# Performance work log

Measured on AMD Instinct MI355X. Metric: run time of the kernel, lower is better.

Reference implementation:

```python
import jax, jax.numpy as jnp
import numpy as np

C = 256          # in_channels == inter_channels (structurally required)
B, H, W = 16, 64, 64


def setup_inputs() -> dict:
    key = jax.random.key(0)
    ks = jax.random.split(key, 10)
    s = 1.0 / np.sqrt(C)
    x = jax.random.normal(ks[0], (B, C, H, W), dtype=jnp.float32)
    # theta / phi: 1x1 convs, stored as [out, in]
    theta_w = jax.random.normal(ks[1], (C, C), dtype=jnp.float32) * s
    theta_b = jax.random.normal(ks[2], (C,), dtype=jnp.float32) * s
    phi_w = jax.random.normal(ks[3], (C, C), dtype=jnp.float32) * s
    phi_b = jax.random.normal(ks[4], (C,), dtype=jnp.float32) * s
    # grouped conv: Conv2d(C, 2C, kernel=(C,1), groups=C).
    # torch weight [2C, 1, C, 1] with group-major out-channel order -> [C groups, 2 per group, C taps]
    gw = jax.random.normal(ks[5], (C, 2, C), dtype=jnp.float32) * s
    gb = jax.random.normal(ks[6], (C, 2), dtype=jnp.float32) * s
    # dim_adjust: 1x1 conv 2C -> C, stored as [C, 2C]
    dw = jax.random.normal(ks[7], (C, 2 * C), dtype=jnp.float32) * (1.0 / np.sqrt(2 * C))
    db = jax.random.normal(ks[8], (C,), dtype=jnp.float32) * (1.0 / np.sqrt(2 * C))
    return {"x": x, "theta_w": theta_w, "theta_b": theta_b,
            "phi_w": phi_w, "phi_b": phi_b,
            "gw": gw, "gb": gb, "dw": dw, "db": db}


def reference(x, theta_w, theta_b, phi_w, phi_b, gw, gb, dw, db):
    b, c, h, w = x.shape
    xf = x.reshape(b, c, h * w)                                   # [B,C,HW]
    theta = jnp.einsum('oc,bcn->bon', theta_w, xf) + theta_b[:, None]  # [B,Ci,HW]
    phi = jnp.einsum('oc,bcn->bon', phi_w, xf) + phi_b[:, None]        # [B,Ci,HW]
    f = jnp.einsum('bon,bpn->bop', theta, phi)                    # [B,Ci,Ci] channel similarity
    # grouped conv: group g sees channel g of f over its 'spatial' axis (length Ci),
    # producing 2 outputs per group via a full-height dot product.
    g = jnp.einsum('bgk,gjk->bgj', f, gw) + gb                    # [B,C,2]
    g = jax.nn.relu(g).reshape(b, 2 * c)                          # [B,2C]
    out = jnp.einsum('bo,co->bc', g, dw) + db                     # [B,C] 1x1 conv
    return out[:, :, None, None]                                  # [B,C,1,1]
```

## Files before the change

### kernel.cpp

```cpp
#include <hip/hip_runtime.h>


#define CC  256
#define NB  16
#define HWN 4096

typedef __attribute__((ext_vector_type(4))) float f32x4;
typedef __attribute__((ext_vector_type(8))) short bf16x8;

__device__ inline unsigned short f2bf(float f) {
  unsigned u = __float_as_uint(f);
  u += 0x7fff + ((u >> 16) & 1);
  return (unsigned short)(u >> 16);
}
__device__ inline float bf2f(unsigned u) { return __uint_as_float(u << 16); }

__global__ __launch_bounds__(1024, 4) void k_gram(const float* __restrict__ x,
                                                  unsigned short* __restrict__ slab,
                                                  float* __restrict__ S) {
  const int ks = blockIdx.x, b = blockIdx.y;
  const float* xb = x + (size_t)b * CC * HWN;
  __shared__ unsigned short As[2][256 * 64];

  const int tid = threadIdx.x, w = tid >> 6, lane = tid & 63;
  const int quad = lane >> 4, m15 = lane & 15;
  const int srow = tid >> 4;
  const int scol = (tid & 15) << 2;
  const int sg = scol >> 3, so = scol & 7;

  f32x4 acc[16];
  #pragma unroll
  for (int i = 0; i < 16; ++i) acc[i] = (f32x4){0.f, 0.f, 0.f, 0.f};
  float rs[4] = {0.f, 0.f, 0.f, 0.f};

  const int k0 = ks * 256;
  float4 ld[4];
  #pragma unroll
  for (int p = 0; p < 4; ++p)
    ld[p] = *(const float4*)(xb + (size_t)(p * 64 + srow) * HWN + k0 + scol);
  #pragma unroll
  for (int p = 0; p < 4; ++p) {
    const int row = p * 64 + srow;
    rs[p] += ld[p].x + ld[p].y + ld[p].z + ld[p].w;
    *(ushort4*)&As[0][row * 64 + ((sg ^ (row & 7)) << 3) + so] =
        make_ushort4(f2bf(ld[p].x), f2bf(ld[p].y), f2bf(ld[p].z), f2bf(ld[p].w));
  }
  __syncthreads();

  #pragma unroll
  for (int i = 0; i < 4; ++i) {
    const int cur = i & 1;
    if (i < 3) {
      const int kc = k0 + (i + 1) * 64;
      #pragma unroll
      for (int p = 0; p < 4; ++p)
        ld[p] = *(const float4*)(xb + (size_t)(p * 64 + srow) * HWN + kc + scol);
    }
    const int rowa = 16 * w + m15;
    #pragma unroll
    for (int kkg = 0; kkg < 8; kkg += 4) {
      const int ga = (kkg + quad) ^ (m15 & 7);
      bf16x8 af = *(const bf16x8*)&As[cur][rowa * 64 + ga * 8];
      #pragma unroll
      for (int ct = 0; ct < 16; ++ct) {
        bf16x8 bfr = *(const bf16x8*)&As[cur][(16 * ct + m15) * 64 + ga * 8];
        acc[ct] = __builtin_amdgcn_mfma_f32_16x16x32_bf16(af, bfr, acc[ct], 0, 0, 0);
      }
    }
    if (i < 3) {
      #pragma unroll
      for (int p = 0; p < 4; ++p) {
        const int row = p * 64 + srow;
        rs[p] += ld[p].x + ld[p].y + ld[p].z + ld[p].w;
        *(ushort4*)&As[1 - cur][row * 64 + ((sg ^ (row & 7)) << 3) + so] =
            make_ushort4(f2bf(ld[p].x), f2bf(ld[p].y), f2bf(ld[p].z), f2bf(ld[p].w));
      }
    }
    __syncthreads();
  }

  unsigned short* sb = slab + ((size_t)(ks * 16 + b) << 16) + w * 4096 + lane;
  #pragma unroll
  for (int ct = 0; ct < 16; ++ct)
    #pragma unroll
    for (int reg = 0; reg < 4; ++reg)
      sb[(ct * 4 + reg) * 64] = f2bf(acc[ct][reg]);

  #pragma unroll
  for (int p = 0; p < 4; ++p) {
    float v = rs[p];
    v += __shfl_xor(v, 1);
    v += __shfl_xor(v, 2);
    v += __shfl_xor(v, 4);
    v += __shfl_xor(v, 8);
    if ((tid & 15) == 0) atomicAdd(&S[b * 256 + p * 64 + srow], v);
  }
}

__global__ __launch_bounds__(256) void k_reduce(const unsigned short* __restrict__ slab,
                                                unsigned short* __restrict__ Gh) {
  const int t = blockIdx.x * 256 + threadIdx.x;
  const int b = t >> 13;
  const int o = (t & 8191) << 3;
  float s[8];
  #pragma unroll
  for (int i = 0; i < 8; ++i) s[i] = 0.f;
  #pragma unroll
  for (int ks = 0; ks < 16; ++ks) {
    const uint4 v = *(const uint4*)(slab + (((size_t)(ks * 16 + b)) << 16) + o);
    s[0] += bf2f(v.x & 0xffffu); s[1] += bf2f(v.x >> 16);
    s[2] += bf2f(v.y & 0xffffu); s[3] += bf2f(v.y >> 16);
    s[4] += bf2f(v.z & 0xffffu); s[5] += bf2f(v.z >> 16);
    s[6] += bf2f(v.w & 0xffffu); s[7] += bf2f(v.w >> 16);
  }
  const int wv = o >> 12, rem = o & 4095;
  const int ctreg = rem >> 6, lane6 = rem & 63;
  const int ct = ctreg >> 2, reg = ctreg & 3;
  const int quad = lane6 >> 4, m0 = lane6 & 15;
  const int row = 16 * wv + 4 * quad + reg;
  const int col = 16 * ct + m0;
  uint4 ov;
  ov.x = (unsigned)f2bf(s[0]) | ((unsigned)f2bf(s[1]) << 16);
  ov.y = (unsigned)f2bf(s[2]) | ((unsigned)f2bf(s[3]) << 16);
  ov.z = (unsigned)f2bf(s[4]) | ((unsigned)f2bf(s[5]) << 16);
  ov.w = (unsigned)f2bf(s[6]) | ((unsigned)f2bf(s[7]) << 16);
  *(uint4*)(Gh + (((size_t)b) << 16) + row * 256 + col) = ov;
}

__global__ __launch_bounds__(256) void k_mid(const float* __restrict__ gw,
                                             const float* __restrict__ pw,
                                             const float* __restrict__ pb,
                                             const float* __restrict__ tw,
                                             const float* __restrict__ S,
                                             unsigned short* __restrict__ Qh,
                                             float* __restrict__ E,
                                             float* __restrict__ U,
                                             float* __restrict__ V) {
  __shared__ float sm[512];
  const int tid = threadIdx.x, blk = blockIdx.x;
  if (blk < 512) {
    const int rj = blk;
    sm[tid] = gw[rj * 256 + tid];
    __syncthreads();
    float q = 0.f;
    for (int p = 0; p < 256; ++p) q += sm[p] * pw[p * 256 + tid];
    Qh[rj * 256 + tid] = f2bf(q);
    sm[256 + tid] = sm[tid] * pb[tid];
    __syncthreads();
    for (int s = 128; s > 0; s >>= 1) {
      if (tid < s) sm[256 + tid] += sm[256 + tid + s];
      __syncthreads();
    }
    if (tid == 0) E[rj] = sm[256];
  } else {
    const int m = blk - 512;
    const int b = m & 15, mat = m >> 4;
    const float* Wm = mat ? pw : tw;
    float* outp = mat ? V : U;
    sm[tid] = S[b * 256 + tid];
    __syncthreads();
    const int l = tid & 15, oh = tid >> 4;
    #pragma unroll
    for (int oc = 0; oc < 16; ++oc) {
      const int o = oc * 16 + oh;
      float a = 0.f;
      #pragma unroll
      for (int j = 0; j < 16; ++j)
        a += Wm[o * 256 + l * 16 + j] * sm[l * 16 + j];
      a += __shfl_xor(a, 1);
      a += __shfl_xor(a, 2);
      a += __shfl_xor(a, 4);
      a += __shfl_xor(a, 8);
      if (l == 0) outp[b * 256 + o] = a;
    }
  }
}

__global__ __launch_bounds__(512) void k_p(const unsigned short* __restrict__ Gh,
                                           const unsigned short* __restrict__ Qh,
                                           const float* __restrict__ tw,
                                           const float* __restrict__ gw,
                                           const float* __restrict__ U,
                                           const float* __restrict__ V,
                                           const float* __restrict__ E,
                                           const float* __restrict__ tb,
                                           const float* __restrict__ gb,
                                           float* __restrict__ GR) {
  const int rjt = blockIdx.x, b = blockIdx.y;
  const int rj0 = rjt * 32;
  const int tid = threadIdx.x, w = tid >> 6, lane = tid & 63;
  const int quad = lane >> 4, m15 = lane & 15;
  const unsigned short* Gb = Gh + ((size_t)b << 16);

  f32x4 acc[2][2];
  #pragma unroll
  for (int mt = 0; mt < 2; ++mt) {
    acc[mt][0] = (f32x4){0.f, 0.f, 0.f, 0.f};
    acc[mt][1] = (f32x4){0.f, 0.f, 0.f, 0.f};
  }

  #pragma unroll
  for (int s = 0; s < 8; ++s) {
    const int kb = s * 32 + quad * 8;
    bf16x8 bq0 = *(const bf16x8*)(Qh + (rj0 + m15) * 256 + kb);
    bf16x8 bq1 = *(const bf16x8*)(Qh + (rj0 + 16 + m15) * 256 + kb);
    #pragma unroll
    for (int mt = 0; mt < 2; ++mt) {
      bf16x8 ag = *(const bf16x8*)(Gb + (32 * w + 16 * mt + m15) * 256 + kb);
      acc[mt][0] = __builtin_amdgcn_mfma_f32_16x16x32_bf16(ag, bq0, acc[mt][0], 0, 0, 0);
      acc[mt][1] = __builtin_amdgcn_mfma_f32_16x16x32_bf16(ag, bq1, acc[mt][1], 0, 0, 0);
    }
  }

  __shared__ float sred[32 * 8];
  __shared__ float sred2[32];
  #pragma unroll
  for (int nt = 0; nt < 2; ++nt) {
    const int rj = rj0 + 16 * nt + m15;
    const int r = rj >> 1;
    float p = 0.f;
    #pragma unroll
    for (int mt = 0; mt < 2; ++mt)
      #pragma unroll
      for (int reg = 0; reg < 4; ++reg)
        p += acc[mt][nt][reg] * tw[r * 256 + 32 * w + 16 * mt + quad * 4 + reg];
    p += __shfl_xor(p, 16);
    p += __shfl_xor(p, 32);
    if (quad == 0) sred[(16 * nt + m15) * 8 + w] = p;
  }
  {
    const int oi = tid >> 4, seg = tid & 15;
    const int rj = rj0 + oi;
    float p2 = 0.f;
    #pragma unroll
    for (int i = 0; i < 16; ++i) {
      const int cp = seg * 16 + i;
      p2 += gw[rj * 256 + cp] * V[b * 256 + cp];
    }
    p2 += __shfl_xor(p2, 1);
    p2 += __shfl_xor(p2, 2);
    p2 += __shfl_xor(p2, 4);
    p2 += __shfl_xor(p2, 8);
    if (seg == 0) sred2[oi] = p2;
  }
  __syncthreads();
  if (tid < 32) {
    const int rj = rj0 + tid, r = rj >> 1;
    float v = 0.f;
    #pragma unroll
    for (int k = 0; k < 8; ++k) v += sred[tid * 8 + k];
    const float tbr = tb[r];
    const float bias = tbr * sred2[tid] +
                       (U[b * 256 + r] + 4096.0f * tbr) * E[rj] + gb[rj];
    GR[b * 512 + rj] = fmaxf(v + bias, 0.f);
  }
}

__global__ __launch_bounds__(256) void k_out(const float* __restrict__ GR,
                                             const float* __restrict__ dw,
                                             const float* __restrict__ db,
                                             float* __restrict__ out) {
  const int cch = blockIdx.x, b = blockIdx.y, tid = threadIdx.x;
  __shared__ float gl[512];
  gl[tid] = GR[b * 512 + tid];
  gl[256 + tid] = GR[b * 512 + 256 + tid];
  __syncthreads();
  const int cl = tid >> 4, l = tid & 15;
  const int c = cch * 16 + cl;
  float a = 0.f;
  #pragma unroll 8
  for (int i = 0; i < 32; ++i) {
    const int o = i * 16 + l;
    a += gl[o] * dw[c * 512 + o];
  }
  a += __shfl_xor(a, 1);
  a += __shfl_xor(a, 2);
  a += __shfl_xor(a, 4);
  a += __shfl_xor(a, 8);
  if (l == 0) out[b * 256 + c] = a + db[c];
}

extern "C" void kernel_launch(void* const* d_in, const int* in_sizes, int n_in,
                              void* d_out, int out_size, void* d_ws, size_t ws_size,
                              hipStream_t stream) {
  const float* x  = (const float*)d_in[0];
  const float* tw = (const float*)d_in[1];
  const float* tb = (const float*)d_in[2];
  const float* pw = (const float*)d_in[3];
  const float* pb = (const float*)d_in[4];
  const float* gw = (const float*)d_in[5];
  const float* gb = (const float*)d_in[6];
  const float* dw = (const float*)d_in[7];
  const float* db = (const float*)d_in[8];
  float* out = (float*)d_out;

  unsigned short* slab = (unsigned short*)d_ws;
  unsigned short* Gh   = slab + ((size_t)256 << 16);
  unsigned short* Qh   = Gh + ((size_t)16 << 16);
  float* S  = (float*)(Qh + 512 * 256);
  float* E  = S + NB * 256;
  float* U  = E + 512;
  float* V  = U + NB * 256;
  float* GR = V + NB * 256;

  hipMemsetAsync(S, 0, NB * 256 * sizeof(float), stream);
  k_gram<<<dim3(16, 16), 1024, 0, stream>>>(x, slab, S);
  k_reduce<<<512, 256, 0, stream>>>(slab, Gh);
  k_mid<<<544, 256, 0, stream>>>(gw, pw, pb, tw, S, Qh, E, U, V);
  k_p<<<dim3(16, NB), 512, 0, stream>>>(Gh, Qh, tw, gw, U, V, E, tb, gb, GR);
  k_out<<<dim3(16, NB), 256, 0, stream>>>(GR, dw, db, out);
}
```

Before: 168.1 us.

## Exploit Gram symmetry, double K-split, and fuse reduce with mid kernel

The Gram kernel now computes only the upper-triangular 16x16 tiles of the symmetric channel matrix, doubles the K-split to 32 chunks so more blocks fill the GPU, and writes compact per-split partials and row sums instead of using atomics. The reduce and mid stages are merged into one launch that also mirrors tiles to rebuild the full matrix, and the memset is dropped. k_p is retiled to smaller blocks with more of them. The gain should come from fewer MFMAs, better occupancy and fewer launches, at the cost of twice as many partial slabs to reduce and wave-level load imbalance in the triangular loop.

```diff
diff --git a/kernel.cpp b/kernel.cpp
--- a/kernel.cpp
+++ b/kernel.cpp
@@ -4,6 +4,8 @@
 #define CC  256
 #define NB  16
 #define HWN 4096
+#define KSPLIT 32
+#define NPAIR 136
 
 typedef __attribute__((ext_vector_type(4))) float f32x4;
 typedef __attribute__((ext_vector_type(8))) short bf16x8;
@@ -17,7 +19,7 @@
 
 __global__ __launch_bounds__(1024, 4) void k_gram(const float* __restrict__ x,
                                                   unsigned short* __restrict__ slab,
-                                                  float* __restrict__ S) {
+                                                  float* __restrict__ Spart) {
   const int ks = blockIdx.x, b = blockIdx.y;
   const float* xb = x + (size_t)b * CC * HWN;
   __shared__ unsigned short As[2][256 * 64];
@@ -33,7 +35,7 @@
   for (int i = 0; i < 16; ++i) acc[i] = (f32x4){0.f, 0.f, 0.f, 0.f};
   float rs[4] = {0.f, 0.f, 0.f, 0.f};
 
-  const int k0 = ks * 256;
+  const int k0 = ks * 128;
   float4 ld[4];
   #pragma unroll
   for (int p = 0; p < 4; ++p)
@@ -48,43 +50,47 @@
   __syncthreads();
 
   #pragma unroll
-  for (int i = 0; i < 4; ++i) {
-    const int cur = i & 1;
-    if (i < 3) {
-      const int kc = k0 + (i + 1) * 64;
+  for (int i = 0; i < 2; ++i) {
+    if (i < 1) {
       #pragma unroll
       for (int p = 0; p < 4; ++p)
-        ld[p] = *(const float4*)(xb + (size_t)(p * 64 + srow) * HWN + kc + scol);
+        ld[p] = *(const float4*)(xb + (size_t)(p * 64 + srow) * HWN + k0 + 64 + scol);
     }
     const int rowa = 16 * w + m15;
     #pragma unroll
     for (int kkg = 0; kkg < 8; kkg += 4) {
       const int ga = (kkg + quad) ^ (m15 & 7);
-      bf16x8 af = *(const bf16x8*)&As[cur][rowa * 64 + ga * 8];
+      bf16x8 af = *(const bf16x8*)&As[i][rowa * 64 + ga * 8];
       #pragma unroll
       for (int ct = 0; ct < 16; ++ct) {
-        bf16x8 bfr = *(const bf16x8*)&As[cur][(16 * ct + m15) * 64 + ga * 8];
+        if (ct < w) continue;
+        bf16x8 bfr = *(const bf16x8*)&As[i][(16 * ct + m15) * 64 + ga * 8];
         acc[ct] = __builtin_amdgcn_mfma_f32_16x16x32_bf16(af, bfr, acc[ct], 0, 0, 0);
       }
     }
-    if (i < 3) {
+    if (i < 1) {
       #pragma unroll
       for (int p = 0; p < 4; ++p) {
         const int row = p * 64 + srow;
         rs[p] += ld[p].x + ld[p].y + ld[p].z + ld[p].w;
-        *(ushort4*)&As[1 - cur][row * 64 + ((sg ^ (row & 7)) << 3) + so] =
+        *(ushort4*)&As[1][row * 64 + ((sg ^ (row & 7)) << 3) + so] =
             make_ushort4(f2bf(ld[p].x), f2bf(ld[p].y), f2bf(ld[p].z), f2bf(ld[p].w));
       }
     }
     __syncthreads();
   }
 
-  unsigned short* sb = slab + ((size_t)(ks * 16 + b) << 16) + w * 4096 + lane;
-  #pragma unroll
-  for (int ct = 0; ct < 16; ++ct)
-    #pragma unroll
-    for (int reg = 0; reg < 4; ++reg)
-      sb[(ct * 4 + reg) * 64] = f2bf(acc[ct][reg]);
+  const int off_w = 16 * w - (w * (w - 1)) / 2;
+  unsigned short* sbase = slab + ((size_t)(ks * 16 + b) * NPAIR) * 256;
+  #pragma unroll
+  for (int ct = 0; ct < 16; ++ct) {
+    if (ct < w) continue;
+    const int pid = off_w + (ct - w);
+    uint2 ov;
+    ov.x = (unsigned)f2bf(acc[ct][0]) | ((unsigned)f2bf(acc[ct][1]) << 16);
+    ov.y = (unsigned)f2bf(acc[ct][2]) | ((unsigned)f2bf(acc[ct][3]) << 16);
+    *(uint2*)(sbase + pid * 256 + lane * 4) = ov;
+  }
 
   #pragma unroll
   for (int p = 0; p < 4; ++p) {
@@ -93,53 +99,55 @@
     v += __shfl_xor(v, 2);
     v += __shfl_xor(v, 4);
     v += __shfl_xor(v, 8);
-    if ((tid & 15) == 0) atomicAdd(&S[b * 256 + p * 64 + srow], v);
-  }
-}
-
-__global__ __launch_bounds__(256) void k_reduce(const unsigned short* __restrict__ slab,
-                                                unsigned short* __restrict__ Gh) {
-  const int t = blockIdx.x * 256 + threadIdx.x;
-  const int b = t >> 13;
-  const int o = (t & 8191) << 3;
-  float s[8];
-  #pragma unroll
-  for (int i = 0; i < 8; ++i) s[i] = 0.f;
-  #pragma unroll
-  for (int ks = 0; ks < 16; ++ks) {
-    const uint4 v = *(const uint4*)(slab + (((size_t)(ks * 16 + b)) << 16) + o);
-    s[0] += bf2f(v.x & 0xffffu); s[1] += bf2f(v.x >> 16);
-    s[2] += bf2f(v.y & 0xffffu); s[3] += bf2f(v.y >> 16);
-    s[4] += bf2f(v.z & 0xffffu); s[5] += bf2f(v.z >> 16);
-    s[6] += bf2f(v.w & 0xffffu); s[7] += bf2f(v.w >> 16);
-  }
-  const int wv = o >> 12, rem = o & 4095;
-  const int ctreg = rem >> 6, lane6 = rem & 63;
-  const int ct = ctreg >> 2, reg = ctreg & 3;
-  const int quad = lane6 >> 4, m0 = lane6 & 15;
-  const int row = 16 * wv + 4 * quad + reg;
-  const int col = 16 * ct + m0;
-  uint4 ov;
-  ov.x = (unsigned)f2bf(s[0]) | ((unsigned)f2bf(s[1]) << 16);
-  ov.y = (unsigned)f2bf(s[2]) | ((unsigned)f2bf(s[3]) << 16);
-  ov.z = (unsigned)f2bf(s[4]) | ((unsigned)f2bf(s[5]) << 16);
-  ov.w = (unsigned)f2bf(s[6]) | ((unsigned)f2bf(s[7]) << 16);
-  *(uint4*)(Gh + (((size_t)b) << 16) + row * 256 + col) = ov;
-}
-
-__global__ __launch_bounds__(256) void k_mid(const float* __restrict__ gw,
-                                             const float* __restrict__ pw,
-                                             const float* __restrict__ pb,
-                                             const float* __restrict__ tw,
-                                             const float* __restrict__ S,
-                                             unsigned short* __restrict__ Qh,
-                                             float* __restrict__ E,
-                                             float* __restrict__ U,
-                                             float* __restrict__ V) {
-  __shared__ float sm[512];
-  const int tid = threadIdx.x, blk = blockIdx.x;
-  if (blk < 512) {
-    const int rj = blk;
+    if ((tid & 15) == 0)
+      Spart[(ks * 16 + b) * 256 + p * 64 + srow] = v;
+  }
+}
+
+__global__ __launch_bounds__(256) void k_fuse1(const unsigned short* __restrict__ slab,
+                                               const float* __restrict__ Spart,
+                                               const float* __restrict__ gw,
+                                               const float* __restrict__ pw,
+                                               const float* __restrict__ pb,
+                                               const float* __restrict__ tw,
+                                               unsigned short* __restrict__ Gh,
+                                               unsigned short* __restrict__ Qh,
+                                               float* __restrict__ E,
+                                               float* __restrict__ U,
+                                               float* __restrict__ V) {
+  const int blk = blockIdx.x, tid = threadIdx.x;
+  if (blk < 544) {
+    const int t = blk * 256 + tid;
+    const int b = t / 8704;
+    const int rem = t % 8704;
+    const int pid0 = rem >> 6, lane = rem & 63;
+    int w = 0, p = pid0;
+    while (p >= 16 - w) { p -= 16 - w; ++w; }
+    const int ct = w + p;
+    const int quad = lane >> 4, m15 = lane & 15;
+    float s[4] = {0.f, 0.f, 0.f, 0.f};
+    const unsigned short* sp = slab + (size_t)(b * NPAIR + pid0) * 256 + lane * 4;
+    #pragma unroll
+    for (int ks = 0; ks < KSPLIT; ++ks) {
+      const uint2 v = *(const uint2*)(sp + (size_t)ks * 16 * NPAIR * 256);
+      s[0] += bf2f(v.x & 0xffffu); s[1] += bf2f(v.x >> 16);
+      s[2] += bf2f(v.y & 0xffffu); s[3] += bf2f(v.y >> 16);
+    }
+    unsigned short h[4];
+    #pragma unroll
+    for (int r = 0; r < 4; ++r) h[r] = f2bf(s[r]);
+    unsigned short* Gb = Gh + ((size_t)b << 16);
+    const int rb = 16 * w + quad * 4;
+    const int col = 16 * ct + m15;
+    #pragma unroll
+    for (int r = 0; r < 4; ++r) Gb[(rb + r) * 256 + col] = h[r];
+    uint2 mv;
+    mv.x = (unsigned)h[0] | ((unsigned)h[1] << 16);
+    mv.y = (unsigned)h[2] | ((unsigned)h[3] << 16);
+    *(uint2*)(Gb + col * 256 + rb) = mv;
+  } else if (blk < 1056) {
+    const int rj = blk - 544;
+    __shared__ float sm[512];
     sm[tid] = gw[rj * 256 + tid];
     __syncthreads();
     float q = 0.f;
@@ -153,11 +161,16 @@
     }
     if (tid == 0) E[rj] = sm[256];
   } else {
-    const int m = blk - 512;
+    const int m = blk - 1056;
     const int b = m & 15, mat = m >> 4;
     const float* Wm = mat ? pw : tw;
     float* outp = mat ? V : U;
-    sm[tid] = S[b * 256 + tid];
+    __shared__ float sm[256];
+    float sv = 0.f;
+    #pragma unroll
+    for (int ks = 0; ks < KSPLIT; ++ks)
+      sv += Spart[(ks * 16 + b) * 256 + tid];
+    sm[tid] = sv;
     __syncthreads();
     const int l = tid & 15, oh = tid >> 4;
     #pragma unroll
@@ -176,7 +189,7 @@
   }
 }
 
-__global__ __launch_bounds__(512) void k_p(const unsigned short* __restrict__ Gh,
+__global__ __launch_bounds__(256) void k_p(const unsigned short* __restrict__ Gh,
                                            const unsigned short* __restrict__ Qh,
                                            const float* __restrict__ tw,
                                            const float* __restrict__ gw,
@@ -187,46 +200,40 @@
                                            const float* __restrict__ gb,
                                            float* __restrict__ GR) {
   const int rjt = blockIdx.x, b = blockIdx.y;
-  const int rj0 = rjt * 32;
+  const int rj0 = rjt * 16;
   const int tid = threadIdx.x, w = tid >> 6, lane = tid & 63;
   const int quad = lane >> 4, m15 = lane & 15;
   const unsigned short* Gb = Gh + ((size_t)b << 16);
 
-  f32x4 acc[2][2];
-  #pragma unroll
-  for (int mt = 0; mt < 2; ++mt) {
-    acc[mt][0] = (f32x4){0.f, 0.f, 0.f, 0.f};
-    acc[mt][1] = (f32x4){0.f, 0.f, 0.f, 0.f};
-  }
+  f32x4 acc[4];
+  #pragma unroll
+  for (int mt = 0; mt < 4; ++mt) acc[mt] = (f32x4){0.f, 0.f, 0.f, 0.f};
 
   #pragma unroll
   for (int s = 0; s < 8; ++s) {
     const int kb = s * 32 + quad * 8;
-    bf16x8 bq0 = *(const bf16x8*)(Qh + (rj0 + m15) * 256 + kb);
-    bf16x8 bq1 = *(const bf16x8*)(Qh + (rj0 + 16 + m15) * 256 + kb);
-    #pragma unroll
-    for (int mt = 0; mt < 2; ++mt) {
-      bf16x8 ag = *(const bf16x8*)(Gb + (32 * w + 16 * mt + m15) * 256 + kb);
-      acc[mt][0] = __builtin_amdgcn_mfma_f32_16x16x32_bf16(ag, bq0, acc[mt][0], 0, 0, 0);
-      acc[mt][1] = __builtin_amdgcn_mfma_f32_16x16x32_bf16(ag, bq1, acc[mt][1], 0, 0, 0);
-    }
-  }
-
-  __shared__ float sred[32 * 8];
-  __shared__ float sred2[32];
-  #pragma unroll
-  for (int nt = 0; nt < 2; ++nt) {
-    const int rj = rj0 + 16 * nt + m15;
+    bf16x8 bq = *(const bf16x8*)(Qh + (rj0 + m15) * 256 + kb);
+    #pragma unroll
+    for (int mt = 0; mt < 4; ++mt) {
+      bf16x8 ag = *(const bf16x8*)(Gb + (64 * w + 16 * mt + m15) * 256 + kb);
+      acc[mt] = __builtin_amdgcn_mfma_f32_16x16x32_bf16(ag, bq, acc[mt], 0, 0, 0);
+    }
+  }
+
+  __shared__ float sred[16 * 4];
+  __shared__ float sred2[16];
+  {
+    const int rj = rj0 + m15;
     const int r = rj >> 1;
     float p = 0.f;
     #pragma unroll
-    for (int mt = 0; mt < 2; ++mt)
+    for (int mt = 0; mt < 4; ++mt)
       #pragma unroll
       for (int reg = 0; reg < 4; ++reg)
-        p += acc[mt][nt][reg] * tw[r * 256 + 32 * w + 16 * mt + quad * 4 + reg];
+        p += acc[mt][reg] * tw[r * 256 + 64 * w + 16 * mt + quad * 4 + reg];
     p += __shfl_xor(p, 16);
     p += __shfl_xor(p, 32);
-    if (quad == 0) sred[(16 * nt + m15) * 8 + w] = p;
+    if (quad == 0) sred[m15 * 4 + w] = p;
   }
   {
     const int oi = tid >> 4, seg = tid & 15;
@@ -244,11 +251,10 @@
     if (seg == 0) sred2[oi] = p2;
   }
   __syncthreads();
-  if (tid < 32) {
+  if (tid < 16) {
     const int rj = rj0 + tid, r = rj >> 1;
-    float v = 0.f;
-    #pragma unroll
-    for (int k = 0; k < 8; ++k) v += sred[tid * 8 + k];
+    const float v = sred[tid * 4] + sred[tid * 4 + 1] +
+                    sred[tid * 4 + 2] + sred[tid * 4 + 3];
     const float tbr = tb[r];
     const float bias = tbr * sred2[tid] +
                        (U[b * 256 + r] + 4096.0f * tbr) * E[rj] + gb[rj];
@@ -295,18 +301,16 @@
   float* out = (float*)d_out;
 
   unsigned short* slab = (unsigned short*)d_ws;
-  unsigned short* Gh   = slab + ((size_t)256 << 16);
+  unsigned short* Gh   = slab + (size_t)KSPLIT * 16 * NPAIR * 256;
   unsigned short* Qh   = Gh + ((size_t)16 << 16);
-  float* S  = (float*)(Qh + 512 * 256);
-  float* E  = S + NB * 256;
+  float* Spart = (float*)(Qh + 512 * 256);
+  float* E  = Spart + KSPLIT * 16 * 256;
   float* U  = E + 512;
   float* V  = U + NB * 256;
   float* GR = V + NB * 256;
 
-  hipMemsetAsync(S, 0, NB * 256 * sizeof(float), stream);
-  k_gram<<<dim3(16, 16), 1024, 0, stream>>>(x, slab, S);
-  k_reduce<<<512, 256, 0, stream>>>(slab, Gh);
-  k_mid<<<544, 256, 0, stream>>>(gw, pw, pb, tw, S, Qh, E, U, V);
-  k_p<<<dim3(16, NB), 512, 0, stream>>>(Gh, Qh, tw, gw, U, V, E, tb, gb, GR);
+  k_gram<<<dim3(KSPLIT, 16), 1024, 0, stream>>>(x, slab, Spart);
+  k_fuse1<<<1088, 256, 0, stream>>>(slab, Spart, gw, pw, pb, tw, Gh, Qh, E, U, V);
+  k_p<<<dim3(32, NB), 256, 0, stream>>>(Gh, Qh, tw, gw, U, V, E, tb, gb, GR);
   k_out<<<dim3(16, NB), 256, 0, stream>>>(GR, dw, db, out);
 }
```

After: 152.2 us. 1.1x faster.
